# Optimization experiments

Measured on AMD Instinct MI355X. Metric: run time of the kernel, lower is better.

Reference implementation:

```python
import jax, jax.numpy as jnp
import numpy as np

N = 6144
HIDDEN = 48
HEADS = 3
HEAD = HIDDEN // HEADS


def setup_inputs() -> dict:
    key = jax.random.key(0)
    ks = jax.random.split(key, 8)
    s = 1.0 / np.sqrt(HIDDEN)
    A = (jax.random.uniform(ks[0], (N, N)) < 0.05).astype(jnp.float32)
    h = jax.random.normal(ks[1], (N, HIDDEN), dtype=jnp.float32)
    Wq = jax.random.normal(ks[2], (HIDDEN, HIDDEN), dtype=jnp.float32) * s
    Wk = jax.random.normal(ks[3], (HIDDEN, HIDDEN), dtype=jnp.float32) * s
    Wv = jax.random.normal(ks[4], (HIDDEN, HIDDEN), dtype=jnp.float32) * s
    bq = jnp.zeros((HIDDEN,), jnp.float32)
    bk = jnp.zeros((HIDDEN,), jnp.float32)
    bv = jnp.zeros((HIDDEN,), jnp.float32)
    return {"A": A, "h": h, "Wq": Wq, "bq": bq, "Wk": Wk, "bk": bk, "Wv": Wv, "bv": bv}


def reference(A, h, Wq, bq, Wk, bk, Wv, bv):
    n = h.shape[0]
    # QKV projections (torch Linear: x @ W.T + b)
    q = (h @ Wq.T + bq).reshape(n, HEADS, HEAD).transpose(1, 0, 2)  # [H,N,d]
    k = (h @ Wk.T + bk).reshape(n, HEADS, HEAD).transpose(1, 0, 2)
    v = (h @ Wv.T + bv).reshape(n, HEADS, HEAD).transpose(1, 0, 2)
    # scores = (q k^T) * A / N**(-0.5)  == (q k^T) * A * sqrt(N)  (faithful to source)
    scale = jnp.asarray(n, h.dtype) ** 0.5
    scores = jnp.einsum("hnd,hmd->hnm", q, k) * A[None, :, :] * scale
    scores = jax.nn.softmax(scores, axis=2)
    out = jnp.einsum("hnm,hmd->hnd", scores, v)  # [H,N,d]
    out = out.transpose(1, 0, 2).reshape(n, HIDDEN)
    return (out, scores)
```

## Files before the change

kernel.cpp:

```cpp
#include <hip/hip_runtime.h>
#include <math.h>

#define NN   6144
#define HID  48
#define BLK  256
#define RPB  4
#define CAP  448
#define CTOT (RPB*CAP)
#define SCALE 78.38367176906175f

typedef float vf4 __attribute__((ext_vector_type(4)));

__global__ __launch_bounds__(256)
void qkv_kernel(const float* __restrict__ h,
                const float* __restrict__ Wq, const float* __restrict__ bq,
                const float* __restrict__ Wk, const float* __restrict__ bk,
                const float* __restrict__ Wv, const float* __restrict__ bv,
                float* __restrict__ qw, float* __restrict__ kw, float* __restrict__ vw) {
    int idx = blockIdx.x * blockDim.x + threadIdx.x;
    int i = idx / HID, c = idx % HID;
    const float4* h4  = (const float4*)(h + (size_t)i * HID);
    const float4* wq4 = (const float4*)(Wq + (size_t)c * HID);
    const float4* wk4 = (const float4*)(Wk + (size_t)c * HID);
    const float4* wv4 = (const float4*)(Wv + (size_t)c * HID);
    float aq = 0.f, ak = 0.f, av = 0.f;
    #pragma unroll
    for (int r = 0; r < HID / 4; ++r) {
        float4 hv = h4[r];
        float4 q4 = wq4[r], k4 = wk4[r], v4 = wv4[r];
        aq = fmaf(hv.x, q4.x, aq); aq = fmaf(hv.y, q4.y, aq);
        aq = fmaf(hv.z, q4.z, aq); aq = fmaf(hv.w, q4.w, aq);
        ak = fmaf(hv.x, k4.x, ak); ak = fmaf(hv.y, k4.y, ak);
        ak = fmaf(hv.z, k4.z, ak); ak = fmaf(hv.w, k4.w, ak);
        av = fmaf(hv.x, v4.x, av); av = fmaf(hv.y, v4.y, av);
        av = fmaf(hv.w, v4.w, av); av = fmaf(hv.z, v4.z, av);
    }
    aq += bq[c]; ak += bk[c]; av += bv[c];
    int head = c >> 4, d = c & 15;
    size_t off = ((size_t)head * NN + i) * 16 + d;
    qw[off] = aq; kw[off] = ak; vw[off] = av;
}

__global__ __launch_bounds__(256)
void vtot_kernel(const float* __restrict__ vw, float* __restrict__ vtot) {
    int c = blockIdx.x;
    int head = c >> 4, d = c & 15;
    float s = 0.f;
    for (int j = threadIdx.x; j < NN; j += 256)
        s += vw[((size_t)head * NN + j) * 16 + d];
    #pragma unroll
    for (int o = 32; o; o >>= 1) s += __shfl_xor(s, o, 64);
    __shared__ float red[4];
    int wid = threadIdx.x >> 6, lane = threadIdx.x & 63;
    if (lane == 0) red[wid] = s;
    __syncthreads();
    if (threadIdx.x == 0) vtot[c] = red[0] + red[1] + red[2] + red[3];
}

__global__ __launch_bounds__(BLK, 4)
void attn_kernel(const float* __restrict__ A,
                 const float* __restrict__ qw, const float* __restrict__ kw,
                 const float* __restrict__ vw, const float* __restrict__ vtot,
                 float* __restrict__ out) {
    __shared__ int   list[CTOT];
    __shared__ float sc[3][CTOT];
    __shared__ __align__(16) float qs[RPB * 48];
    __shared__ unsigned pmM[RPB][BLK];
    __shared__ unsigned short pmB[RPB][BLK];
    __shared__ float wredML[4 * 12 * 2];
    __shared__ float MF[12], ZF[12], IVF[12];
    __shared__ unsigned wlo[4], whi[4];

    const int i0 = blockIdx.x * RPB;
    const int tid = threadIdx.x;
    const int wid = tid >> 6, lane = tid & 63;

    if (tid < RPB * 48) {
        int r = tid / 48, c = tid % 48;
        int hh = c >> 4, d = c & 15;
        qs[tid] = qw[((size_t)hh * NN + (i0 + r)) * 16 + d];
    }

    unsigned mr[RPB];
    #pragma unroll
    for (int r = 0; r < RPB; ++r) {
        const vf4* Ar = (const vf4*)(A + (size_t)(i0 + r) * NN);
        unsigned mm = 0u;
        #pragma unroll
        for (int c = 0; c < 6; ++c) {
            vf4 a4 = __builtin_nontemporal_load(&Ar[tid + c * BLK]);
            int p = c * 4;
            if (a4.x != 0.f) mm |= 1u << (p + 0);
            if (a4.y != 0.f) mm |= 1u << (p + 1);
            if (a4.z != 0.f) mm |= 1u << (p + 2);
            if (a4.w != 0.f) mm |= 1u << (p + 3);
        }
        mr[r] = mm;
    }
    unsigned lo = (unsigned)__popc(mr[0]) | ((unsigned)__popc(mr[1]) << 16);
    unsigned hi = (unsigned)__popc(mr[2]) | ((unsigned)__popc(mr[3]) << 16);

    unsigned ilo = lo, ihi = hi;
    #pragma unroll
    for (int o = 1; o < 64; o <<= 1) {
        unsigned plo = __shfl_up(ilo, o, 64);
        unsigned phi = __shfl_up(ihi, o, 64);
        if (lane >= o) { ilo += plo; ihi += phi; }
    }
    if (lane == 63) { wlo[wid] = ilo; whi[wid] = ihi; }
    __syncthreads();
    unsigned blo = ilo - lo, bhi = ihi - hi;
    unsigned tlo = 0, thi = 0;
    #pragma unroll
    for (int w = 0; w < 4; ++w) {
        unsigned a = wlo[w], b = whi[w];
        if (w < wid) { blo += a; bhi += b; }
        tlo += a; thi += b;
    }
    const int C0 = min((int)(tlo & 0xFFFFu), CAP), C1 = min((int)(tlo >> 16), CAP);
    const int C2 = min((int)(thi & 0xFFFFu), CAP), C3 = min((int)(thi >> 16), CAP);
    const int cum1 = C0, cum2 = C0 + C1, cum3 = cum2 + C2;
    int bs[4] = {(int)(blo & 0xFFFFu), (int)(blo >> 16),
                 (int)(bhi & 0xFFFFu), (int)(bhi >> 16)};
    int cu[5] = {0, cum1, cum2, cum3, cum3 + C3};

    #pragma unroll
    for (int r = 0; r < RPB; ++r) {
        pmM[r][tid] = mr[r];
        pmB[r][tid] = (unsigned short)bs[r];
    }

    #pragma unroll
    for (int r = 0; r < RPB; ++r) {
        unsigned m = mr[r];
        int b = bs[r];
        while (m) {
            int p = __ffs(m) - 1; m &= m - 1;
            if (b < CAP) list[cu[r] + b] = 4 * (tid + (p >> 2) * BLK) + (p & 3);
            ++b;
        }
    }
    __syncthreads();

    {
        const int q4 = tid >> 2, part = tid & 3;
        #pragma unroll
        for (int r = 0; r < RPB; ++r) {
            float4 qv0 = ((const float4*)(qs + r * 48 +  0))[part];
            float4 qv1 = ((const float4*)(qs + r * 48 + 16))[part];
            float4 qv2 = ((const float4*)(qs + r * 48 + 32))[part];
            float mA = 0.f, lA = 0.f, mB = 0.f, lB = 0.f, mC = 0.f, lC = 0.f;
            for (int e = cu[r] + q4; e < cu[r + 1]; e += (BLK >> 2)) {
                int j = list[e];
                float4 k0 = ((const float4*)(kw + ((size_t)0 * NN + j) * 16))[part];
                float4 k1 = ((const float4*)(kw + ((size_t)1 * NN + j) * 16))[part];
                float4 k2 = ((const float4*)(kw + ((size_t)2 * NN + j) * 16))[part];
                float d0 = k0.x * qv0.x; d0 = fmaf(k0.y, qv0.y, d0);
                d0 = fmaf(k0.z, qv0.z, d0); d0 = fmaf(k0.w, qv0.w, d0);
                float d1 = k1.x * qv1.x; d1 = fmaf(k1.y, qv1.y, d1);
                d1 = fmaf(k1.z, qv1.z, d1); d1 = fmaf(k1.w, qv1.w, d1);
                float d2 = k2.x * qv2.x; d2 = fmaf(k2.y, qv2.y, d2);
                d2 = fmaf(k2.z, qv2.z, d2); d2 = fmaf(k2.w, qv2.w, d2);
                d0 += __shfl_xor(d0, 1, 64); d0 += __shfl_xor(d0, 2, 64);
                d1 += __shfl_xor(d1, 1, 64); d1 += __shfl_xor(d1, 2, 64);
                d2 += __shfl_xor(d2, 1, 64); d2 += __shfl_xor(d2, 2, 64);
                float s0 = d0 * SCALE, s1 = d1 * SCALE, s2 = d2 * SCALE;
                if (part == 0) sc[0][e] = s0;
                else if (part == 1) sc[1][e] = s1;
                else if (part == 2) sc[2][e] = s2;
                float nm;
                nm = fmaxf(mA, s0); lA = lA * __expf(mA - nm) + __expf(s0 - nm); mA = nm;
                nm = fmaxf(mB, s1); lB = lB * __expf(mB - nm) + __expf(s1 - nm); mB = nm;
                nm = fmaxf(mC, s2); lC = lC * __expf(mC - nm) + __expf(s2 - nm); mC = nm;
            }
            #pragma unroll
            for (int o = 4; o < 64; o <<= 1) {
                float om, ol, nm;
                om = __shfl_xor(mA, o, 64); ol = __shfl_xor(lA, o, 64);
                nm = fmaxf(mA, om); lA = lA * __expf(mA - nm) + ol * __expf(om - nm); mA = nm;
                om = __shfl_xor(mB, o, 64); ol = __shfl_xor(lB, o, 64);
                nm = fmaxf(mB, om); lB = lB * __expf(mB - nm) + ol * __expf(om - nm); mB = nm;
                om = __shfl_xor(mC, o, 64); ol = __shfl_xor(lC, o, 64);
                nm = fmaxf(mC, om); lC = lC * __expf(mC - nm) + ol * __expf(om - nm); mC = nm;
            }
            if (lane == 0) {
                int b0 = (wid * 12 + r * 3) * 2;
                wredML[b0 + 0] = mA; wredML[b0 + 1] = lA;
                wredML[b0 + 2] = mB; wredML[b0 + 3] = lB;
                wredML[b0 + 4] = mC; wredML[b0 + 5] = lC;
            }
        }
    }
    __syncthreads();

    if (tid < 12) {
        int r = tid / 3;
        int Cr = (r == 0) ? C0 : (r == 1) ? C1 : (r == 2) ? C2 : C3;
        float M = wredML[tid * 2], L = wredML[tid * 2 + 1];
        #pragma unroll
        for (int w = 1; w < 4; ++w) {
            float mw = wredML[(w * 12 + tid) * 2], lw = wredML[(w * 12 + tid) * 2 + 1];
            float nm = fmaxf(M, mw);
            L = L * __expf(M - nm) + lw * __expf(mw - nm);
            M = nm;
        }
        float z = __expf(-M);
        MF[tid] = M; ZF[tid] = z;
        IVF[tid] = 1.0f / (L + (float)(NN - Cr) * z);
    }
    __syncthreads();

    if (wid == 0) {
        const int rr4 = lane & 3, a = lane >> 2;
        #pragma unroll
        for (int h = 0; h < 3; ++h) {
            const float* vbase = vw + (size_t)h * NN * 16 + rr4 * 4;
            #pragma unroll
            for (int r = 0; r < RPB; ++r) {
                int s = r * 3 + h;
                float M = MF[s], zz = ZF[s], iv = IVF[s];
                float ax = 0.f, ay = 0.f, az = 0.f, aw = 0.f;
                #pragma unroll 2
                for (int e = cu[r] + a; e < cu[r + 1]; e += 16) {
                    float p = __expf(sc[h][e] - M);
                    float w = p - zz;
                    int j = list[e];
                    float4 vv = *(const float4*)(vbase + (size_t)j * 16);
                    ax = fmaf(w, vv.x, ax); ay = fmaf(w, vv.y, ay);
                    az = fmaf(w, vv.z, az); aw = fmaf(w, vv.w, aw);
                }
                #pragma unroll
                for (int o = 4; o < 64; o <<= 1) {
                    ax += __shfl_xor(ax, o, 64); ay += __shfl_xor(ay, o, 64);
                    az += __shfl_xor(az, o, 64); aw += __shfl_xor(aw, o, 64);
                }
                if (a == 0) {
                    int c0 = h * 16 + rr4 * 4;
                    float4 vt = *(const float4*)(vtot + c0);
                    float4 o4;
                    o4.x = (ax + zz * vt.x) * iv;
                    o4.y = (ay + zz * vt.y) * iv;
                    o4.z = (az + zz * vt.z) * iv;
                    o4.w = (aw + zz * vt.w) * iv;
                    *(float4*)(out + (size_t)(i0 + r) * HID + c0) = o4;
                }
            }
        }
    } else {
        float* Pp = out + (size_t)NN * HID;
        const size_t NSQ = (size_t)NN * NN;
        const int t = tid - 64;
        #pragma unroll
        for (int r = 0; r < RPB; ++r) {
            int s = r * 3;
            float M0 = MF[s], M1 = MF[s + 1], M2 = MF[s + 2];
            float iv0 = IVF[s], iv1 = IVF[s + 1], iv2 = IVF[s + 2];
            float zi0 = ZF[s] * iv0, zi1 = ZF[s + 1] * iv1, zi2 = ZF[s + 2] * iv2;
            size_t rowoff = (size_t)(i0 + r) * NN;
            #pragma unroll 2
            for (int p = t; p < NN / 4; p += 192) {
                unsigned msk = pmM[r][p & (BLK - 1)];
                int c = p >> 8;
                unsigned nib = (msk >> (c * 4)) & 0xFu;
                int idx = (int)pmB[r][p & (BLK - 1)] + __popc(msk & ((1u << (c * 4)) - 1u));
                vf4 P0, P1, P2;
                #pragma unroll
                for (int e = 0; e < 4; ++e) {
                    int nz = (int)((nib >> e) & 1u);
                    if (nz && idx < CAP) {
                        int slot = cu[r] + idx;
                        P0[e] = __expf(sc[0][slot] - M0) * iv0;
                        P1[e] = __expf(sc[1][slot] - M1) * iv1;
                        P2[e] = __expf(sc[2][slot] - M2) * iv2;
                    } else { P0[e] = zi0; P1[e] = zi1; P2[e] = zi2; }
                    idx += nz;
                }
                __builtin_nontemporal_store(P0, &((vf4*)(Pp + rowoff))[p]);
                __builtin_nontemporal_store(P1, &((vf4*)(Pp + NSQ + rowoff))[p]);
                __builtin_nontemporal_store(P2, &((vf4*)(Pp + 2 * NSQ + rowoff))[p]);
            }
        }
    }
}

extern "C" void kernel_launch(void* const* d_in, const int* in_sizes, int n_in,
                              void* d_out, int out_size, void* d_ws, size_t ws_size,
                              hipStream_t stream) {
    const float* A  = (const float*)d_in[0];
    const float* h  = (const float*)d_in[1];
    const float* Wq = (const float*)d_in[2];
    const float* bq = (const float*)d_in[3];
    const float* Wk = (const float*)d_in[4];
    const float* bk = (const float*)d_in[5];
    const float* Wv = (const float*)d_in[6];
    const float* bv = (const float*)d_in[7];
    float* out = (float*)d_out;
    float* ws  = (float*)d_ws;

    float* qw   = ws;
    float* kw   = ws + (size_t)3 * NN * 16;
    float* vw   = ws + (size_t)6 * NN * 16;
    float* vtot = ws + (size_t)9 * NN * 16;

    qkv_kernel<<<(NN * HID) / 256, 256, 0, stream>>>(h, Wq, bq, Wk, bk, Wv, bv, qw, kw, vw);
    vtot_kernel<<<HID, 256, 0, stream>>>(vw, vtot);
    attn_kernel<<<NN / RPB, BLK, 0, stream>>>(A, qw, kw, vw, vtot, out);
}
```

Before: 624.9 us.

## Halve rows per block and let all threads write probabilities from register masks

Drops rows per block from 4 to 2 and raises launch bounds to 8 blocks per CU, so there are more, smaller blocks. The P-matrix write-out no longer uses a dedicated 192-thread group reading shared mask tables. Every thread now writes the columns it loaded, using its register mask and prefix offset, which removes the pmM/pmB shared arrays. The A·V accumulation is spread across three waves (one per head) instead of one. The cost is more blocks, tighter register limits, and waves 0-2 doing the AV work before they join the P writes.

```diff
diff --git a/kernel.cpp b/kernel.cpp
--- a/kernel.cpp
+++ b/kernel.cpp
@@ -4,10 +4,11 @@
 #define NN   6144
 #define HID  48
 #define BLK  256
-#define RPB  4
+#define RPB  2
 #define CAP  448
 #define CTOT (RPB*CAP)
 #define SCALE 78.38367176906175f
+#define NBLK (NN/RPB)
 
 typedef float vf4 __attribute__((ext_vector_type(4)));
 
@@ -57,7 +58,7 @@
     if (threadIdx.x == 0) vtot[c] = red[0] + red[1] + red[2] + red[3];
 }
 
-__global__ __launch_bounds__(BLK, 4)
+__global__ __launch_bounds__(BLK, 8)
 void attn_kernel(const float* __restrict__ A,
                  const float* __restrict__ qw, const float* __restrict__ kw,
                  const float* __restrict__ vw, const float* __restrict__ vtot,
@@ -65,11 +66,9 @@
     __shared__ int   list[CTOT];
     __shared__ float sc[3][CTOT];
     __shared__ __align__(16) float qs[RPB * 48];
-    __shared__ unsigned pmM[RPB][BLK];
-    __shared__ unsigned short pmB[RPB][BLK];
-    __shared__ float wredML[4 * 12 * 2];
-    __shared__ float MF[12], ZF[12], IVF[12];
-    __shared__ unsigned wlo[4], whi[4];
+    __shared__ float wredML[4 * 6 * 2];
+    __shared__ float MF[6], ZF[6], IVF[6];
+    __shared__ unsigned wsc[4];
 
     const int i0 = blockIdx.x * RPB;
     const int tid = threadIdx.x;
@@ -98,37 +97,26 @@
         mr[r] = mm;
     }
     unsigned lo = (unsigned)__popc(mr[0]) | ((unsigned)__popc(mr[1]) << 16);
-    unsigned hi = (unsigned)__popc(mr[2]) | ((unsigned)__popc(mr[3]) << 16);
-
-    unsigned ilo = lo, ihi = hi;
+
+    unsigned il = lo;
     #pragma unroll
     for (int o = 1; o < 64; o <<= 1) {
-        unsigned plo = __shfl_up(ilo, o, 64);
-        unsigned phi = __shfl_up(ihi, o, 64);
-        if (lane >= o) { ilo += plo; ihi += phi; }
-    }
-    if (lane == 63) { wlo[wid] = ilo; whi[wid] = ihi; }
-    __syncthreads();
-    unsigned blo = ilo - lo, bhi = ihi - hi;
-    unsigned tlo = 0, thi = 0;
+        unsigned pl = __shfl_up(il, o, 64);
+        if (lane >= o) il += pl;
+    }
+    if (lane == 63) wsc[wid] = il;
+    __syncthreads();
+    unsigned bl = il - lo, tl = 0;
     #pragma unroll
     for (int w = 0; w < 4; ++w) {
-        unsigned a = wlo[w], b = whi[w];
-        if (w < wid) { blo += a; bhi += b; }
-        tlo += a; thi += b;
-    }
-    const int C0 = min((int)(tlo & 0xFFFFu), CAP), C1 = min((int)(tlo >> 16), CAP);
-    const int C2 = min((int)(thi & 0xFFFFu), CAP), C3 = min((int)(thi >> 16), CAP);
-    const int cum1 = C0, cum2 = C0 + C1, cum3 = cum2 + C2;
-    int bs[4] = {(int)(blo & 0xFFFFu), (int)(blo >> 16),
-                 (int)(bhi & 0xFFFFu), (int)(bhi >> 16)};
-    int cu[5] = {0, cum1, cum2, cum3, cum3 + C3};
-
-    #pragma unroll
-    for (int r = 0; r < RPB; ++r) {
-        pmM[r][tid] = mr[r];
-        pmB[r][tid] = (unsigned short)bs[r];
-    }
+        unsigned a = wsc[w];
+        if (w < wid) bl += a;
+        tl += a;
+    }
+    const int C0 = min((int)(tl & 0xFFFFu), CAP), C1 = min((int)(tl >> 16), CAP);
+    int Cr2[2] = {C0, C1};
+    int cu[3] = {0, C0, C0 + C1};
+    int bs[2] = {(int)(bl & 0xFFFFu), (int)(bl >> 16)};
 
     #pragma unroll
     for (int r = 0; r < RPB; ++r) {
@@ -184,7 +172,7 @@
                 nm = fmaxf(mC, om); lC = lC * __expf(mC - nm) + ol * __expf(om - nm); mC = nm;
             }
             if (lane == 0) {
-                int b0 = (wid * 12 + r * 3) * 2;
+                int b0 = (wid * 6 + r * 3) * 2;
                 wredML[b0 + 0] = mA; wredML[b0 + 1] = lA;
                 wredML[b0 + 2] = mB; wredML[b0 + 3] = lB;
                 wredML[b0 + 4] = mC; wredML[b0 + 5] = lC;
@@ -193,92 +181,86 @@
     }
     __syncthreads();
 
-    if (tid < 12) {
+    if (tid < 6) {
         int r = tid / 3;
-        int Cr = (r == 0) ? C0 : (r == 1) ? C1 : (r == 2) ? C2 : C3;
         float M = wredML[tid * 2], L = wredML[tid * 2 + 1];
         #pragma unroll
         for (int w = 1; w < 4; ++w) {
-            float mw = wredML[(w * 12 + tid) * 2], lw = wredML[(w * 12 + tid) * 2 + 1];
+            float mw = wredML[(w * 6 + tid) * 2], lw = wredML[(w * 6 + tid) * 2 + 1];
             float nm = fmaxf(M, mw);
             L = L * __expf(M - nm) + lw * __expf(mw - nm);
             M = nm;
         }
         float z = __expf(-M);
         MF[tid] = M; ZF[tid] = z;
-        IVF[tid] = 1.0f / (L + (float)(NN - Cr) * z);
-    }
-    __syncthreads();
-
-    if (wid == 0) {
-        const int rr4 = lane & 3, a = lane >> 2;
-        #pragma unroll
-        for (int h = 0; h < 3; ++h) {
-            const float* vbase = vw + (size_t)h * NN * 16 + rr4 * 4;
+        IVF[tid] = 1.0f / (L + (float)(NN - Cr2[r]) * z);
+    }
+    __syncthreads();
+
+    if (wid < 3) {
+        const int h = wid, rr4 = lane & 3, a = lane >> 2;
+        const float* vbase = vw + (size_t)h * NN * 16 + rr4 * 4;
+        #pragma unroll
+        for (int r = 0; r < RPB; ++r) {
+            int s = r * 3 + h;
+            float M = MF[s], zz = ZF[s], iv = IVF[s];
+            float ax = 0.f, ay = 0.f, az = 0.f, aw = 0.f;
+            #pragma unroll 2
+            for (int e = cu[r] + a; e < cu[r + 1]; e += 16) {
+                float p = __expf(sc[h][e] - M);
+                float w = p - zz;
+                int j = list[e];
+                float4 vv = *(const float4*)(vbase + (size_t)j * 16);
+                ax = fmaf(w, vv.x, ax); ay = fmaf(w, vv.y, ay);
+                az = fmaf(w, vv.z, az); aw = fmaf(w, vv.w, aw);
+            }
             #pragma unroll
-            for (int r = 0; r < RPB; ++r) {
-                int s = r * 3 + h;
-                float M = MF[s], zz = ZF[s], iv = IVF[s];
-                float ax = 0.f, ay = 0.f, az = 0.f, aw = 0.f;
-                #pragma unroll 2
-                for (int e = cu[r] + a; e < cu[r + 1]; e += 16) {
-                    float p = __expf(sc[h][e] - M);
-                    float w = p - zz;
-                    int j = list[e];
-                    float4 vv = *(const float4*)(vbase + (size_t)j * 16);
-                    ax = fmaf(w, vv.x, ax); ay = fmaf(w, vv.y, ay);
-                    az = fmaf(w, vv.z, az); aw = fmaf(w, vv.w, aw);
-                }
-                #pragma unroll
-                for (int o = 4; o < 64; o <<= 1) {
-                    ax += __shfl_xor(ax, o, 64); ay += __shfl_xor(ay, o, 64);
-                    az += __shfl_xor(az, o, 64); aw += __shfl_xor(aw, o, 64);
-                }
-                if (a == 0) {
-                    int c0 = h * 16 + rr4 * 4;
-                    float4 vt = *(const float4*)(vtot + c0);
-                    float4 o4;
-                    o4.x = (ax + zz * vt.x) * iv;
-                    o4.y = (ay + zz * vt.y) * iv;
-                    o4.z = (az + zz * vt.z) * iv;
-                    o4.w = (aw + zz * vt.w) * iv;
-                    *(float4*)(out + (size_t)(i0 + r) * HID + c0) = o4;
-                }
-            }
-        }
-    } else {
-        float* Pp = out + (size_t)NN * HID;
-        const size_t NSQ = (size_t)NN * NN;
-        const int t = tid - 64;
-        #pragma unroll
-        for (int r = 0; r < RPB; ++r) {
-            int s = r * 3;
-            float M0 = MF[s], M1 = MF[s + 1], M2 = MF[s + 2];
-            float iv0 = IVF[s], iv1 = IVF[s + 1], iv2 = IVF[s + 2];
-            float zi0 = ZF[s] * iv0, zi1 = ZF[s + 1] * iv1, zi2 = ZF[s + 2] * iv2;
-            size_t rowoff = (size_t)(i0 + r) * NN;
-            #pragma unroll 2
-            for (int p = t; p < NN / 4; p += 192) {
-                unsigned msk = pmM[r][p & (BLK - 1)];
-                int c = p >> 8;
-                unsigned nib = (msk >> (c * 4)) & 0xFu;
-                int idx = (int)pmB[r][p & (BLK - 1)] + __popc(msk & ((1u << (c * 4)) - 1u));
-                vf4 P0, P1, P2;
-                #pragma unroll
-                for (int e = 0; e < 4; ++e) {
-                    int nz = (int)((nib >> e) & 1u);
-                    if (nz && idx < CAP) {
-                        int slot = cu[r] + idx;
-                        P0[e] = __expf(sc[0][slot] - M0) * iv0;
-                        P1[e] = __expf(sc[1][slot] - M1) * iv1;
-                        P2[e] = __expf(sc[2][slot] - M2) * iv2;
-                    } else { P0[e] = zi0; P1[e] = zi1; P2[e] = zi2; }
-                    idx += nz;
-                }
-                __builtin_nontemporal_store(P0, &((vf4*)(Pp + rowoff))[p]);
-                __builtin_nontemporal_store(P1, &((vf4*)(Pp + NSQ + rowoff))[p]);
-                __builtin_nontemporal_store(P2, &((vf4*)(Pp + 2 * NSQ + rowoff))[p]);
-            }
+            for (int o = 4; o < 64; o <<= 1) {
+                ax += __shfl_xor(ax, o, 64); ay += __shfl_xor(ay, o, 64);
+                az += __shfl_xor(az, o, 64); aw += __shfl_xor(aw, o, 64);
+            }
+            if (a == 0) {
+                int c0 = h * 16 + rr4 * 4;
+                float4 vt = *(const float4*)(vtot + c0);
+                float4 o4;
+                o4.x = (ax + zz * vt.x) * iv;
+                o4.y = (ay + zz * vt.y) * iv;
+                o4.z = (az + zz * vt.z) * iv;
+                o4.w = (aw + zz * vt.w) * iv;
+                *(float4*)(out + (size_t)(i0 + r) * HID + c0) = o4;
+            }
+        }
+    }
+
+    float* Pp = out + (size_t)NN * HID;
+    const size_t NSQ = (size_t)NN * NN;
+    #pragma unroll
+    for (int r = 0; r < RPB; ++r) {
+        int s = r * 3;
+        float M0 = MF[s], M1 = MF[s + 1], M2 = MF[s + 2];
+        float iv0 = IVF[s], iv1 = IVF[s + 1], iv2 = IVF[s + 2];
+        float zi0 = ZF[s] * iv0, zi1 = ZF[s + 1] * iv1, zi2 = ZF[s + 2] * iv2;
+        size_t rowoff = (size_t)(i0 + r) * NN;
+        unsigned msk = mr[r];
+        #pragma unroll
+        for (int c = 0; c < 6; ++c) {
+            unsigned nib = (msk >> (c * 4)) & 0xFu;
+            int idx = bs[r] + __popc(msk & ((1u << (c * 4)) - 1u));
+            vf4 P0, P1, P2;
+            #pragma unroll
+            for (int e = 0; e < 4; ++e) {
+                int nz = (int)((nib >> e) & 1u);
+                if (nz && idx < CAP) {
+                    int slot = cu[r] + idx;
+                    P0[e] = __expf(sc[0][slot] - M0) * iv0;
+                    P1[e] = __expf(sc[1][slot] - M1) * iv1;
+                    P2[e] = __expf(sc[2][slot] - M2) * iv2;
+                } else { P0[e] = zi0; P1[e] = zi1; P2[e] = zi2; }
+                idx += nz;
+            }
+            __builtin_nontemporal_store(P0, &((vf4*)(Pp + rowoff))[tid + c * BLK]);
+            __builtin_nontemporal_store(P1, &((vf4*)(Pp + NSQ + rowoff))[tid + c * BLK]);
+            __builtin_nontemporal_store(P2, &((vf4*)(Pp + 2 * NSQ + rowoff))[tid + c * BLK]);
         }
     }
 }
@@ -304,5 +286,5 @@
 
     qkv_kernel<<<(NN * HID) / 256, 256, 0, stream>>>(h, Wq, bq, Wk, bk, Wv, bv, qw, kw, vw);
     vtot_kernel<<<HID, 256, 0, stream>>>(vw, vtot);
-    attn_kernel<<<NN / RPB, BLK, 0, stream>>>(A, qw, kw, vw, vtot, out);
-}
+    attn_kernel<<<NBLK, BLK, 0, stream>>>(A, qw, kw, vw, vtot, out);
+}
```

After: 627.2 us. No clear change (+0.4%).
